# Optimization experiments

Measured on AMD Instinct MI355X. Metric: run time of the kernel, lower is better.

Reference implementation:

```python
import jax, jax.numpy as jnp
import numpy as np

NUM_HEADS = 16
NEG_INF = -9000000000000000.0


def setup_inputs() -> dict:
    key = jax.random.key(0)
    ks = jax.random.split(key, 4)
    B, S, D = 2, 2048, 1024
    x = jax.random.normal(ks[0], (B, S, D), dtype=jnp.float32)
    mask = jax.random.randint(ks[1], (1, 1, S, S), 0, 2, dtype=jnp.int32)
    # xavier-uniform-ish init scaled down for stability
    w_qkv = jax.random.normal(ks[2], (3 * D, D), dtype=jnp.float32) * (1.0 / np.sqrt(D))
    b_qkv = jnp.zeros((3 * D,), dtype=jnp.float32)
    w_o = jax.random.normal(ks[3], (D, D), dtype=jnp.float32) * (1.0 / np.sqrt(D))
    b_o = jnp.zeros((D,), dtype=jnp.float32)
    return {"x": x, "mask": mask, "w_qkv": w_qkv, "b_qkv": b_qkv, "w_o": w_o, "b_o": b_o}


def reference(x, mask, w_qkv, b_qkv, w_o, b_o):
    B, S, D = x.shape
    H = NUM_HEADS
    hd = D // H
    # qkv projection: torch Linear is x @ W.T + b
    qkv = x @ w_qkv.T + b_qkv                      # [B, S, 3D]
    qkv = qkv.reshape(B, S, H, 3 * hd).transpose(0, 2, 1, 3)  # [B, H, S, 3hd]
    q, k, v = jnp.split(qkv, 3, axis=-1)           # each [B, H, S, hd]
    scale = 1.0 / np.sqrt(hd).astype(np.float32)
    logits = jnp.einsum("bhqd,bhkd->bhqk", q, k) * scale  # [B, H, S, S]
    logits = jnp.where(mask == 0, NEG_INF, logits)
    attn = jax.nn.softmax(logits, axis=-1)
    ctx = jnp.einsum("bhqk,bhkd->bhqd", attn, v)   # [B, H, S, hd]
    ctx = ctx.transpose(0, 2, 1, 3).reshape(B, S, D)
    return ctx @ w_o.T + b_o
```

## Files before the change

kernel.cpp:

```cpp
#include <hip/hip_runtime.h>

typedef __attribute__((ext_vector_type(8))) short short8;
typedef __attribute__((ext_vector_type(4))) float f32x4;

#define MFMA16(a, b, c) __builtin_amdgcn_mfma_f32_16x16x32_bf16(a, b, c, 0, 0, 0)

#define BATCH 2
#define SEQ 2048
#define DMODEL 1024
#define NHEADS 16
#define HDIM 64
#define MROWS (BATCH * SEQ)
#define N_QKV (3 * DMODEL)

#define QSCALE 0.1803368801111184f

#define GLDS16(gp, lp)                                                       \
  __builtin_amdgcn_global_load_lds(                                          \
      (const __attribute__((address_space(1))) void*)(gp),                   \
      (__attribute__((address_space(3))) void*)(lp), 16, 0, 0)

#define CFENCE() asm volatile("" ::: "memory")

static __device__ __forceinline__ unsigned short f2bf(float f) {
  unsigned int u = __float_as_uint(f);
  u = (u + 0x7fff + ((u >> 16) & 1)) >> 16;
  return (unsigned short)u;
}

static __device__ __forceinline__ unsigned int pk2bf(float lo, float hi) {
  unsigned int r;
  asm("v_cvt_pk_bf16_f32 %0, %1, %2" : "=v"(r) : "v"(lo), "v"(hi));
  return r;
}

static __device__ __forceinline__ float fexp2(float x) {
  float r;
  asm("v_exp_f32 %0, %1" : "=v"(r) : "v"(x));
  return r;
}

__global__ void prep_kernel(const int* __restrict__ mask,
                            unsigned int* __restrict__ bits,
                            const float* __restrict__ a, unsigned short* __restrict__ oa,
                            int na4, const float* __restrict__ b,
                            unsigned short* __restrict__ ob, int nb4,
                            const float* __restrict__ c,
                            unsigned short* __restrict__ oc, int nc4) {
  if (blockIdx.x < (SEQ * SEQ) / 256) {
    int i = blockIdx.x * 256 + threadIdx.x;
    unsigned long long bl = __ballot(mask[i] != 0);
    if ((threadIdx.x & 63) == 0)
      ((unsigned long long*)bits)[i >> 6] = bl;
    return;
  }
  int j = (blockIdx.x - (SEQ * SEQ) / 256) * 256 + threadIdx.x;
  const float* src;
  unsigned short* dst;
  if (j < na4) {
    src = a; dst = oa;
  } else if ((j -= na4) < nb4) {
    src = b; dst = ob;
  } else if ((j -= nb4) < nc4) {
    src = c; dst = oc;
  } else
    return;
  f32x4 v = ((const f32x4*)src)[j];
  ushort4 o;
  o.x = f2bf(v[0]); o.y = f2bf(v[1]); o.z = f2bf(v[2]); o.w = f2bf(v[3]);
  ((ushort4*)dst)[j] = o;
}

template <int EPI, int BM>
__global__ __launch_bounds__(256, 3) void gemm_bt(
    const unsigned short* __restrict__ A, const unsigned short* __restrict__ Bm,
    const float* __restrict__ bias, int Kdim, int Ndim,
    unsigned short* __restrict__ qb, unsigned short* __restrict__ kb,
    unsigned short* __restrict__ vtb, float* __restrict__ Cout) {
  constexpr int WM = (BM == 128) ? 64 : 32;
  constexpr int NI = WM / 16;
  __shared__ __align__(16) unsigned short lA[3][BM * 32];
  __shared__ __align__(16) unsigned short lB[3][128 * 32];

  int t = threadIdx.x;
  int nwg = gridDim.x * gridDim.y;
  int lin = blockIdx.y * gridDim.x + blockIdx.x;
  int swb = (lin & 7) * (nwg >> 3) + (lin >> 3);
  int m0 = (swb / gridDim.x) * BM, n0 = (swb % gridDim.x) * 128;

  int w = t >> 6, lane = t & 63, quad = lane >> 4, l16 = lane & 15;
  int wm = (w >> 1) * WM, wn = (w & 1) * 64;

  f32x4 acc[NI][4];
#pragma unroll
  for (int i = 0; i < NI; ++i)
#pragma unroll
    for (int j = 0; j < 4; ++j) acc[i][j] = (f32x4){0.f, 0.f, 0.f, 0.f};

  int nK = Kdim >> 5;

#define GSTAGE(buf, kk)                                                      \
  do {                                                                       \
    _Pragma("unroll")                                                        \
    for (int c = 0; c < BM / 64; ++c) {                                      \
      int id = t + c * 256;                                                  \
      int row = id >> 2;                                                     \
      int gc = ((id & 3) ^ (row & 3)) << 3; \
      GLDS16(&A[(size_t)(m0 + row) * Kdim + ((kk) << 5) + gc],               \
             (char*)lA[buf] + (id & ~63) * 16);                              \
    }                                                                        \
    _Pragma("unroll")                                                        \
    for (int c = 0; c < 2; ++c) {                                            \
      int id = t + c * 256;                                                  \
      int row = id >> 2;                                                     \
      int gc = ((id & 3) ^ (row & 3)) << 3;                                  \
      GLDS16(&Bm[(size_t)(n0 + row) * Kdim + ((kk) << 5) + gc],              \
             (char*)lB[buf] + (id & ~63) * 16);                              \
    }                                                                        \
  } while (0)

  GSTAGE(0, 0);
  GSTAGE(1, 1);
  int stage = 2;
  for (int kk = 0; kk < nK; ++kk) {
    int cur = kk % 3;
    if (kk + 2 < nK) {
      GSTAGE(stage, kk + 2);
      stage = (stage + 1) % 3;
      if (BM == 128)
        asm volatile("s_waitcnt vmcnt(8)" ::: "memory");
      else
        asm volatile("s_waitcnt vmcnt(6)" ::: "memory");
    } else if (kk + 1 < nK) {
      if (BM == 128)
        asm volatile("s_waitcnt vmcnt(4)" ::: "memory");
      else
        asm volatile("s_waitcnt vmcnt(3)" ::: "memory");
    } else {
      asm volatile("s_waitcnt vmcnt(0)" ::: "memory");
    }
    __builtin_amdgcn_s_barrier();
    CFENCE();
    __builtin_amdgcn_sched_barrier(0);

    short8 af[NI], bfr[4];
    int rswz = (l16 & 3) << 4;
#pragma unroll
    for (int i = 0; i < NI; ++i)
      af[i] = *(const short8*)((const char*)&lA[cur][(wm + i * 16 + l16) * 32] +
                               ((quad * 16) ^ rswz));
#pragma unroll
    for (int j = 0; j < 4; ++j)
      bfr[j] = *(const short8*)((const char*)&lB[cur][(wn + j * 16 + l16) * 32] +
                                ((quad * 16) ^ rswz));
#pragma unroll
    for (int i = 0; i < NI; ++i)
#pragma unroll
      for (int j = 0; j < 4; ++j) acc[i][j] = MFMA16(af[i], bfr[j], acc[i][j]);

    asm volatile("s_waitcnt lgkmcnt(0)" ::: "memory");
    __builtin_amdgcn_s_barrier();
    CFENCE();
  }

#pragma unroll
  for (int j = 0; j < 4; ++j) {
    int n = n0 + wn + j * 16 + l16;
    float bs = bias[n];
    int h = n / 192, rr = n % 192;
#pragma unroll
    for (int i = 0; i < NI; ++i) {
      int mb_ = m0 + wm + i * 16 + quad * 4;
      if (EPI == 0) {
        int b = mb_ >> 11, s = mb_ & 2047;
        int bh = (b << 4) + h;
        if (rr < 64) {
#pragma unroll
          for (int r = 0; r < 4; ++r)
            qb[((size_t)bh * SEQ + s + r) * HDIM + rr] =
                f2bf((acc[i][j][r] + bs) * QSCALE);
        } else if (rr < 128) {
#pragma unroll
          for (int r = 0; r < 4; ++r)
            kb[((size_t)bh * SEQ + s + r) * HDIM + (rr - 64)] =
                f2bf(acc[i][j][r] + bs);
        } else {
          ushort4 u;
          u.x = f2bf(acc[i][j][0] + bs);
          u.y = f2bf(acc[i][j][1] + bs);
          u.z = f2bf(acc[i][j][2] + bs);
          u.w = f2bf(acc[i][j][3] + bs);
          *(ushort4*)&vtb[((size_t)bh * HDIM + (rr - 128)) * SEQ + s] = u;
        }
      } else {
#pragma unroll
        for (int r = 0; r < 4; ++r)
          Cout[(size_t)(mb_ + r) * Ndim + n] = acc[i][j][r] + bs;
      }
    }
  }
}

__global__ __launch_bounds__(256, 2) void attn_kernel(
    const unsigned short* __restrict__ qbuf, const unsigned short* __restrict__ kbuf,
    const unsigned short* __restrict__ vtbuf, const unsigned int* __restrict__ mbits,
    unsigned short* __restrict__ ctx) {
  __shared__ __align__(16) unsigned short lK[2][64 * 64];
  __shared__ __align__(16) unsigned short lV[2][64 * 64];
  __shared__ __align__(16) unsigned short lP[128 * 64];

  int lin = blockIdx.y * gridDim.x + blockIdx.x;
  int slin = (lin & 7) * 64 + (lin >> 3);
  int qt = slin & 15, bh = slin >> 4;
  int q0 = qt * 128;
  const unsigned short* Q = qbuf + (size_t)bh * SEQ * HDIM;
  const unsigned short* K = kbuf + (size_t)bh * SEQ * HDIM;
  const unsigned short* VT = vtbuf + (size_t)bh * HDIM * SEQ;

  int t = threadIdx.x;
  int w = t >> 6, lane = t & 63, quad = lane >> 4, l16 = lane & 15;
  int swz = (l16 & 7) << 4;

  int qr0 = q0 + w * 32 + l16;
  short8 qf[2][2];
#pragma unroll
  for (int mt = 0; mt < 2; ++mt)
#pragma unroll
    for (int kh = 0; kh < 2; ++kh)
      qf[mt][kh] =
          *(const short8*)&Q[(size_t)(qr0 + mt * 16) * HDIM + kh * 32 + quad * 8];

  const short one = (short)0x3F80;
  short8 ones = {one, one, one, one, one, one, one, one};

  f32x4 o[2][4];
#pragma unroll
  for (int mt = 0; mt < 2; ++mt)
#pragma unroll
    for (int jt = 0; jt < 4; ++jt) o[mt][jt] = (f32x4){0.f, 0.f, 0.f, 0.f};
  f32x4 li4[2];
  li4[0] = (f32x4){0.f, 0.f, 0.f, 0.f};
  li4[1] = (f32x4){0.f, 0.f, 0.f, 0.f};

  int scol = ((lane & 7) ^ (lane >> 3)) << 3;
  const unsigned short* gK = K + (size_t)(w * 8 + (lane >> 3)) * HDIM + scol;
  const unsigned short* gV = VT + (size_t)(w * 8 + (lane >> 3)) * SEQ + scol;

#define STAGE_KV(buf)                                            \
  do {                                                           \
    GLDS16(gK, &lK[buf][(w * 8) * 64]);                          \
    GLDS16(gK + 32 * HDIM, &lK[buf][(32 + w * 8) * 64]);         \
    GLDS16(gV, &lV[buf][(w * 8) * 64]);                          \
    GLDS16(gV + 32 * SEQ, &lV[buf][(32 + w * 8) * 64]);          \
  } while (0)

  STAGE_KV(0);
  gK += 64 * HDIM;
  gV += 64;

  const unsigned int* mrow0 = mbits + (size_t)qr0 * 64;
  const unsigned int* mrow1 = mbits + (size_t)(qr0 + 16) * 64;
  unsigned short* lPr0 = &lP[(w * 32 + l16) * 64];
  unsigned short* lPr1 = &lP[(w * 32 + 16 + l16) * 64];

  for (int it = 0; it < SEQ / 64; ++it) {
    __syncthreads();
    if (it + 1 < SEQ / 64) {
      STAGE_KV((it + 1) & 1);
      gK += 64 * HDIM;
      gV += 64;
    }
    const unsigned short* cK = lK[it & 1];
    const unsigned short* cV = lV[it & 1];

    uint2 mw0 = *(const uint2*)&mrow0[it * 2];
    uint2 mw1 = *(const uint2*)&mrow1[it * 2];

    f32x4 s[2][4];
    __builtin_amdgcn_s_setprio(1);
#pragma unroll
    for (int j = 0; j < 4; ++j) {
      const char* kr = (const char*)&cK[(j * 16 + l16) * 64];
      short8 ka = *(const short8*)(kr + ((quad * 16) ^ swz));
      short8 kc = *(const short8*)(kr + ((64 + quad * 16) ^ swz));
#pragma unroll
      for (int mt = 0; mt < 2; ++mt) {
        f32x4 z = (f32x4){0.f, 0.f, 0.f, 0.f};
        z = MFMA16(ka, qf[mt][0], z);
        z = MFMA16(kc, qf[mt][1], z);
        s[mt][j] = z;
      }
    }
    __builtin_amdgcn_s_setprio(0);

#pragma unroll
    for (int mt = 0; mt < 2; ++mt) {
      unsigned int ma = (mt ? mw1.x : mw0.x) >> (quad * 4);
      unsigned int mb = (mt ? mw1.y : mw0.y) >> (quad * 4);
#pragma unroll
      for (int j = 0; j < 4; ++j) {
        unsigned int sel = (j < 2) ? ma : mb;
        int sh = (j & 1) << 4;
#pragma unroll
        for (int r = 0; r < 4; ++r) {
          float v = (sel & (1u << (sh + r))) ? s[mt][j][r] : -1e30f;
          s[mt][j][r] = fexp2(v);
        }
      }
    }

#pragma unroll
    for (int j = 0; j < 4; ++j) {
      uint2 u0, u1;
      u0.x = pk2bf(s[0][j][0], s[0][j][1]);
      u0.y = pk2bf(s[0][j][2], s[0][j][3]);
      u1.x = pk2bf(s[1][j][0], s[1][j][1]);
      u1.y = pk2bf(s[1][j][2], s[1][j][3]);
      *(uint2*)((char*)lPr0 + ((j * 32 + quad * 8) ^ swz)) = u0;
      *(uint2*)((char*)lPr1 + ((j * 32 + quad * 8) ^ swz)) = u1;
    }

    __builtin_amdgcn_s_setprio(1);
#pragma unroll
    for (int kh = 0; kh < 2; ++kh) {
      short8 pf0 = *(const short8*)((const char*)lPr0 + ((kh * 64 + quad * 16) ^ swz));
      short8 pf1 = *(const short8*)((const char*)lPr1 + ((kh * 64 + quad * 16) ^ swz));
      li4[0] = MFMA16(ones, pf0, li4[0]);
      li4[1] = MFMA16(ones, pf1, li4[1]);
#pragma unroll
      for (int jt = 0; jt < 4; ++jt) {
        const char* vr = (const char*)&cV[(jt * 16 + l16) * 64];
        short8 vf = *(const short8*)(vr + ((kh * 64 + quad * 16) ^ swz));
        o[0][jt] = MFMA16(vf, pf0, o[0][jt]);
        o[1][jt] = MFMA16(vf, pf1, o[1][jt]);
      }
    }
    __builtin_amdgcn_s_setprio(0);
  }

  int b = bh >> 4, h = bh & 15;
#pragma unroll
  for (int mt = 0; mt < 2; ++mt) {
    float inv = 1.0f / li4[mt][0];
    unsigned short* crow =
        ctx + ((size_t)(b * SEQ + qr0 + mt * 16)) * DMODEL + h * HDIM;
#pragma unroll
    for (int jt = 0; jt < 4; ++jt) {
      uint2 u;
      u.x = pk2bf(o[mt][jt][0] * inv, o[mt][jt][1] * inv);
      u.y = pk2bf(o[mt][jt][2] * inv, o[mt][jt][3] * inv);
      *(uint2*)&crow[jt * 16 + quad * 4] = u;
    }
  }
}

extern "C" void kernel_launch(void* const* d_in, const int* in_sizes, int n_in,
                              void* d_out, int out_size, void* d_ws, size_t ws_size,
                              hipStream_t stream) {
  const float* x = (const float*)d_in[0];
  const int* mask = (const int*)d_in[1];
  const float* w_qkv = (const float*)d_in[2];
  const float* b_qkv = (const float*)d_in[3];
  const float* w_o = (const float*)d_in[4];
  const float* b_o = (const float*)d_in[5];
  float* out = (float*)d_out;

  char* ws = (char*)d_ws;
  unsigned short* xb = (unsigned short*)(ws);
  unsigned short* wqkvb = (unsigned short*)(ws + (8ull << 20));
  unsigned short* wob = (unsigned short*)(ws + (14ull << 20));
  unsigned short* qb = (unsigned short*)(ws + (16ull << 20));
  unsigned short* kb = (unsigned short*)(ws + (24ull << 20));
  unsigned short* vtb = (unsigned short*)(ws + (32ull << 20));
  unsigned short* ctx = (unsigned short*)(ws + (40ull << 20));
  unsigned int* mbits = (unsigned int*)(ws + (48ull << 20));

  const int na4 = (MROWS * DMODEL) / 4;
  const int nb4 = (N_QKV * DMODEL) / 4;
  const int nc4 = (DMODEL * DMODEL) / 4;
  const int nmask = (SEQ * SEQ) / 256;
  const int ncvt = (na4 + nb4 + nc4 + 255) / 256;
  prep_kernel<<<nmask + ncvt, 256, 0, stream>>>(mask, mbits, x, xb, na4,
                                                w_qkv, wqkvb, nb4, w_o, wob, nc4);

  gemm_bt<0, 128><<<dim3(N_QKV / 128, MROWS / 128), 256, 0, stream>>>(
      xb, wqkvb, b_qkv, DMODEL, N_QKV, qb, kb, vtb, nullptr);

  attn_kernel<<<dim3(SEQ / 128, BATCH * NHEADS), 256, 0, stream>>>(
      qb, kb, vtb, mbits, ctx);

  gemm_bt<1, 64><<<dim3(DMODEL / 128, MROWS / 64), 256, 0, stream>>>(
      ctx, wob, b_o, DMODEL, DMODEL, nullptr, nullptr, nullptr, out);
}
```

Baseline: 213.7 us.

## Shrink GEMM tiles to BN=64 and switch to double-buffered LDS pipeline

Adds a BN template parameter so both projection GEMMs use 64-wide N tiles, doubling the grid size, and drops the triple-buffered LDS ring for a double buffer. Occupancy launch bounds are raised to 4-5 waves per SIMD. The aim is more workgroups across the CUs and lower LDS/register use per block. In exchange each block reuses its data less and has only one stage of prefetch lookahead to hide memory latency.

```diff
diff --git a/kernel.cpp b/kernel.cpp
--- a/kernel.cpp
+++ b/kernel.cpp
@@ -71,31 +71,34 @@
   ((ushort4*)dst)[j] = o;
 }
 
-template <int EPI, int BM>
-__global__ __launch_bounds__(256, 3) void gemm_bt(
+template <int EPI, int BM, int BN>
+__global__ __launch_bounds__(256, (BM + BN == 192) ? 5 : 4) void gemm_bt(
     const unsigned short* __restrict__ A, const unsigned short* __restrict__ Bm,
     const float* __restrict__ bias, int Kdim, int Ndim,
     unsigned short* __restrict__ qb, unsigned short* __restrict__ kb,
     unsigned short* __restrict__ vtb, float* __restrict__ Cout) {
   constexpr int WM = (BM == 128) ? 64 : 32;
+  constexpr int WN = (BN == 128) ? 64 : 32;
   constexpr int NI = WM / 16;
-  __shared__ __align__(16) unsigned short lA[3][BM * 32];
-  __shared__ __align__(16) unsigned short lB[3][128 * 32];
+  constexpr int NJ = WN / 16;
+  constexpr int NLD = BM / 64 + BN / 64;
+  __shared__ __align__(16) unsigned short lA[2][BM * 32];
+  __shared__ __align__(16) unsigned short lB[2][BN * 32];
 
   int t = threadIdx.x;
   int nwg = gridDim.x * gridDim.y;
   int lin = blockIdx.y * gridDim.x + blockIdx.x;
   int swb = (lin & 7) * (nwg >> 3) + (lin >> 3);
-  int m0 = (swb / gridDim.x) * BM, n0 = (swb % gridDim.x) * 128;
+  int m0 = (swb / gridDim.x) * BM, n0 = (swb % gridDim.x) * BN;
 
   int w = t >> 6, lane = t & 63, quad = lane >> 4, l16 = lane & 15;
-  int wm = (w >> 1) * WM, wn = (w & 1) * 64;
-
-  f32x4 acc[NI][4];
+  int wm = (w >> 1) * WM, wn = (w & 1) * WN;
+
+  f32x4 acc[NI][NJ];
 #pragma unroll
   for (int i = 0; i < NI; ++i)
 #pragma unroll
-    for (int j = 0; j < 4; ++j) acc[i][j] = (f32x4){0.f, 0.f, 0.f, 0.f};
+    for (int j = 0; j < NJ; ++j) acc[i][j] = (f32x4){0.f, 0.f, 0.f, 0.f};
 
   int nK = Kdim >> 5;
 
@@ -110,7 +113,7 @@
              (char*)lA[buf] + (id & ~63) * 16);                              \
     }                                                                        \
     _Pragma("unroll")                                                        \
-    for (int c = 0; c < 2; ++c) {                                            \
+    for (int c = 0; c < BN / 64; ++c) {                                      \
       int id = t + c * 256;                                                  \
       int row = id >> 2;                                                     \
       int gc = ((id & 3) ^ (row & 3)) << 3;                                  \
@@ -120,22 +123,16 @@
   } while (0)
 
   GSTAGE(0, 0);
-  GSTAGE(1, 1);
-  int stage = 2;
   for (int kk = 0; kk < nK; ++kk) {
-    int cur = kk % 3;
-    if (kk + 2 < nK) {
-      GSTAGE(stage, kk + 2);
-      stage = (stage + 1) % 3;
-      if (BM == 128)
-        asm volatile("s_waitcnt vmcnt(8)" ::: "memory");
+    int cur = kk & 1;
+    if (kk + 1 < nK) {
+      GSTAGE(cur ^ 1, kk + 1);
+      if constexpr (NLD == 2)
+        asm volatile("s_waitcnt vmcnt(2)" ::: "memory");
+      else if constexpr (NLD == 3)
+        asm volatile("s_waitcnt vmcnt(3)" ::: "memory");
       else
-        asm volatile("s_waitcnt vmcnt(6)" ::: "memory");
-    } else if (kk + 1 < nK) {
-      if (BM == 128)
         asm volatile("s_waitcnt vmcnt(4)" ::: "memory");
-      else
-        asm volatile("s_waitcnt vmcnt(3)" ::: "memory");
     } else {
       asm volatile("s_waitcnt vmcnt(0)" ::: "memory");
     }
@@ -143,20 +140,20 @@
     CFENCE();
     __builtin_amdgcn_sched_barrier(0);
 
-    short8 af[NI], bfr[4];
+    short8 af[NI], bfr[NJ];
     int rswz = (l16 & 3) << 4;
 #pragma unroll
     for (int i = 0; i < NI; ++i)
       af[i] = *(const short8*)((const char*)&lA[cur][(wm + i * 16 + l16) * 32] +
                                ((quad * 16) ^ rswz));
 #pragma unroll
-    for (int j = 0; j < 4; ++j)
+    for (int j = 0; j < NJ; ++j)
       bfr[j] = *(const short8*)((const char*)&lB[cur][(wn + j * 16 + l16) * 32] +
                                 ((quad * 16) ^ rswz));
 #pragma unroll
     for (int i = 0; i < NI; ++i)
 #pragma unroll
-      for (int j = 0; j < 4; ++j) acc[i][j] = MFMA16(af[i], bfr[j], acc[i][j]);
+      for (int j = 0; j < NJ; ++j) acc[i][j] = MFMA16(af[i], bfr[j], acc[i][j]);
 
     asm volatile("s_waitcnt lgkmcnt(0)" ::: "memory");
     __builtin_amdgcn_s_barrier();
@@ -164,7 +161,7 @@
   }
 
 #pragma unroll
-  for (int j = 0; j < 4; ++j) {
+  for (int j = 0; j < NJ; ++j) {
     int n = n0 + wn + j * 16 + l16;
     float bs = bias[n];
     int h = n / 192, rr = n % 192;
@@ -383,12 +380,12 @@
   prep_kernel<<<nmask + ncvt, 256, 0, stream>>>(mask, mbits, x, xb, na4,
                                                 w_qkv, wqkvb, nb4, w_o, wob, nc4);
 
-  gemm_bt<0, 128><<<dim3(N_QKV / 128, MROWS / 128), 256, 0, stream>>>(
+  gemm_bt<0, 128, 64><<<dim3(N_QKV / 64, MROWS / 128), 256, 0, stream>>>(
       xb, wqkvb, b_qkv, DMODEL, N_QKV, qb, kb, vtb, nullptr);
 
   attn_kernel<<<dim3(SEQ / 128, BATCH * NHEADS), 256, 0, stream>>>(
       qb, kb, vtb, mbits, ctx);
 
-  gemm_bt<1, 64><<<dim3(DMODEL / 128, MROWS / 64), 256, 0, stream>>>(
+  gemm_bt<1, 64, 64><<<dim3(DMODEL / 64, MROWS / 64), 256, 0, stream>>>(
       ctx, wob, b_o, DMODEL, DMODEL, nullptr, nullptr, nullptr, out);
 }
```

New measurement: 222.6 us. 1.04x slower.
